# Performance work log

Hardware: AMD Instinct MI355X
Metric: run time of the kernel (lower is better)

Reference implementation:

```python
import jax, jax.numpy as jnp
import numpy as np
import itertools, math

CUTOFF = 10.0
ON_CUT = 0.25 * CUTOFF
OFF_CUT = 0.75 * CUTOFF
ALPHA = 4.0 / CUTOFF + 0.001
ALPHA2 = ALPHA ** 2
TWO_PI = 2.0 * math.pi
ONE_OVER_SQRTPI = 1.0 / math.sqrt(math.pi)
B = 512      # molecules
NA = 128     # atoms per molecule
N = B * NA   # total atoms
DEG = 64     # neighbors per atom
P = N * DEG  # total pairs


def _make_kvecs(Nmax=(2, 2, 2)):
    ks = []
    for i in range(3):
        kk = list(range(Nmax[i] + 1)) + [-v for v in range(1, Nmax[i] + 1)]
        ks.append(kk)
    lk = list(itertools.product(*ks))[1:]  # drop (0,0,0)
    kv = np.array(lk, dtype=np.float32)
    kmax = max(Nmax)
    return jnp.asarray(kv[(kv ** 2).sum(-1) <= kmax ** 2])  # [32,3]


def setup_inputs() -> dict:
    key = jax.random.key(0)
    k1, k2, k3, k4, k5, k6 = jax.random.split(key, 6)
    Z = jax.random.randint(k1, (N,), 1, 94)
    Qa = 0.2 * jax.random.normal(k2, (N,), dtype=jnp.float32)
    R = 20.0 * jax.random.uniform(k3, (N, 3), dtype=jnp.float32)
    Dij = 0.5 + 9.5 * jax.random.uniform(k4, (P,), dtype=jnp.float32)
    idx_i = jnp.repeat(jnp.arange(N), DEG)
    idx_j = (idx_i // NA) * NA + jax.random.randint(k5, (P,), 0, NA)
    batch_seg = jnp.repeat(jnp.arange(B), NA)
    Cell = jnp.tile(20.0 * jnp.eye(3, dtype=jnp.float32), (B, 1, 1)) \
           + 0.05 * jax.random.normal(k6, (B, 3, 3), dtype=jnp.float32)
    kvecs = _make_kvecs()
    return dict(Dij=Dij, Qa=Qa, R=R, Cell=Cell, kvecs=kvecs,
                Z=Z, idx_i=idx_i, idx_j=idx_j, batch_seg=batch_seg)


def _switch_function(x):
    # infinitely smooth switch from 1 (x<=on) to 0 (x>=off)
    def comp(t):
        t_ = jnp.where(t <= 0, 1.0, t)
        return jnp.where(t <= 0, 0.0, jnp.exp(-1.0 / t_))
    x = (x - ON_CUT) / (OFF_CUT - ON_CUT)
    fp = comp(x)
    fm = comp(1.0 - x)
    return jnp.where(x <= 0, 1.0, jnp.where(x >= 1, 0.0, fm / (fp + fm)))


def reference(Dij, Qa, R, Cell, kvecs, Z, idx_i, idx_j, batch_seg):
    # ---- real space: gather -> elementwise -> segment_sum ----
    fac = Qa[idx_i] * Qa[idx_j]                              # [P]
    f = _switch_function(Dij)
    coulomb = 1.0 / Dij
    damped = 1.0 / jnp.sqrt(Dij * Dij + 1.0)
    pw = fac * (f * damped + (1.0 - f) * coulomb) * jax.lax.erfc(ALPHA * Dij)
    e_real = 0.5 * jax.ops.segment_sum(pw, idx_i, num_segments=N)  # [N]

    # ---- reciprocal space ----
    recip_box = TWO_PI * jnp.transpose(jnp.linalg.inv(Cell), (0, 2, 1))  # [B,3,3]
    v_box = jnp.abs(jnp.linalg.det(Cell))                    # [B]
    prefactor = TWO_PI / v_box                               # [B]
    k = jnp.einsum('kx,bxy->bky', kvecs, recip_box)          # [B,K,3]
    k2 = jnp.sum(k * k, axis=-1)                             # [B,K]
    qg = jnp.exp(-0.25 * k2 / ALPHA2)                        # [B,K]
    kd = jnp.einsum('nkx,nx->nk', k[batch_seg], R)           # [N,K]
    q_real = jax.ops.segment_sum(Qa[:, None] * jnp.cos(kd), batch_seg, num_segments=B)  # [B,K]
    q_imag = jax.ops.segment_sum(Qa[:, None] * jnp.sin(kd), batch_seg, num_segments=B)  # [B,K]
    q_dens = q_real ** 2 + q_imag ** 2
    # NOTE: faithful to TF source: reduce over ALL axes -> scalar, then * prefactor [B]
    e_reciprocal = prefactor * jnp.sum(q_dens * qg / k2)     # [B]
    e_self = -ALPHA * ONE_OVER_SQRTPI * jax.ops.segment_sum(Qa * Qa, batch_seg, num_segments=B)
    QaR = jax.ops.segment_sum(Qa[:, None] * R, batch_seg, num_segments=B)  # [B,3]
    e_bc = prefactor / 3.0 * jnp.sum(QaR * QaR, axis=-1)     # [B]
    e_rec_tot = e_reciprocal + e_self + e_bc                 # [B]

    Na_per_batch = jax.ops.segment_sum(jnp.ones_like(batch_seg, dtype=Qa.dtype),
                                       batch_seg, num_segments=B)
    er = (e_rec_tot / Na_per_batch)[batch_seg]               # per-atom broadcast [N]
    return e_real + er, Qa
```

## Files before the change

### kernel.cpp

```cpp
#include <hip/hip_runtime.h>
#include <math.h>

#define ON_CUT_C   2.5f
#define OFF_CUT_C  7.5f
#define ALPHA_C    0.401f
#define ALPHA2_C   0.160801f
#define TWO_PI_C   6.2831853071795864f
#define INV_SQRT_PI_C 0.56418958354775628f
#define NB   512
#define NA_C 128
#define NTOT (NB*NA_C)
#define DEG_C 64
#define KC   32
#define NPTS 1024
#define TSCALE (1024.0f / 9.5f)

#define RCP(x) __builtin_amdgcn_rcpf(x)
#define RSQ(x) __builtin_amdgcn_rsqf(x)


__device__ __forceinline__ float fast_erfc(float x) {
    float t = RCP(1.0f + 0.3275911f * x);
    float p = t*(0.254829592f + t*(-0.284496736f +
              t*(1.421413741f + t*(-1.453152027f + t*1.061405429f))));
    return p * __expf(-x*x);
}

__device__ __forceinline__ float pair_g(float D) {
    float x  = (D - ON_CUT_C) * (1.0f / (OFF_CUT_C - ON_CUT_C));
    float xc = fminf(fmaxf(x, 1e-12f), 0.99999994f);
    float gg = RCP(1.0f - xc) - RCP(xc);
    float f  = RCP(1.0f + __expf(gg));
    float coulomb = RCP(D);
    float damped  = RSQ(D*D + 1.0f);
    return (f*damped + (1.0f - f)*coulomb) * fast_erfc(ALPHA_C * D);
}

__global__ __launch_bounds__(256) void recip_kernel(
    const float* __restrict__ Qa, const float* __restrict__ R,
    const float* __restrict__ Cell, const float* __restrict__ kvecs,
    float* __restrict__ ws)
{
    int b   = blockIdx.x;
    int tid = threadIdx.x;

    __shared__ float4 sar[NA_C];
    __shared__ float skx[KC], sky[KC], skz[KC], sgok2[KC];
    __shared__ float pr[KC][9], pi[KC][9];
    __shared__ float redw[2][4];
    __shared__ float s_pref;

    if (tid < NA_C) {
        int n = b * NA_C + tid;
        sar[tid] = make_float4(Qa[n], R[n*3+0], R[n*3+1], R[n*3+2]);
    }
    if (tid < KC) {
        const float* C = Cell + b * 9;
        float c00=C[0], c01=C[1], c02=C[2];
        float c10=C[3], c11=C[4], c12=C[5];
        float c20=C[6], c21=C[7], c22=C[8];
        float m00 = c11*c22 - c12*c21;
        float m01 = c02*c21 - c01*c22;
        float m02 = c01*c12 - c02*c11;
        float m10 = c12*c20 - c10*c22;
        float m11 = c00*c22 - c02*c20;
        float m12 = c02*c10 - c00*c12;
        float m20 = c10*c21 - c11*c20;
        float m21 = c01*c20 - c00*c21;
        float m22 = c00*c11 - c01*c10;
        float det = c00*m00 + c01*m10 + c02*m20;
        float invdet = 1.0f / det;
        float kv0 = kvecs[tid*3+0], kv1 = kvecs[tid*3+1], kv2 = kvecs[tid*3+2];
        float kx = TWO_PI_C * invdet * (m00*kv0 + m01*kv1 + m02*kv2);
        float ky = TWO_PI_C * invdet * (m10*kv0 + m11*kv1 + m12*kv2);
        float kz = TWO_PI_C * invdet * (m20*kv0 + m21*kv1 + m22*kv2);
        float k2 = kx*kx + ky*ky + kz*kz;
        skx[tid] = kx; sky[tid] = ky; skz[tid] = kz;
        sgok2[tid] = __expf(-0.25f * k2 / ALPHA2_C) / k2;
        if (tid == 0) s_pref = TWO_PI_C / fabsf(det);
    }
    __syncthreads();

    {
        int k = tid & 31, chunk = tid >> 5;
        float kx = skx[k], ky = sky[k], kz = skz[k];
        float cr = 0.0f, ci = 0.0f;
        int a0 = chunk * 16;
        #pragma unroll
        for (int i = 0; i < 16; ++i) {
            float4 ar = sar[a0 + i];
            float kd = kx*ar.y + ky*ar.z + kz*ar.w;
            float s, c;
            __sincosf(kd, &s, &c);
            cr += ar.x * c;
            ci += ar.x * s;
        }
        pr[k][chunk] = cr; pi[k][chunk] = ci;
    }

    if (tid < NA_C) {
        float4 ar = sar[tid];
        float q2 = ar.x*ar.x, px = ar.x*ar.y, py = ar.x*ar.z, pz = ar.x*ar.w;
        #pragma unroll
        for (int off = 32; off; off >>= 1) {
            q2 += __shfl_down(q2, off, 64);
            px += __shfl_down(px, off, 64);
            py += __shfl_down(py, off, 64);
            pz += __shfl_down(pz, off, 64);
        }
        if ((tid & 63) == 0) {
            int w = tid >> 6;
            redw[w][0]=q2; redw[w][1]=px; redw[w][2]=py; redw[w][3]=pz;
        }
    }
    __syncthreads();

    if (tid < KC) {
        float r = 0.0f, im = 0.0f;
        #pragma unroll
        for (int c = 0; c < 8; ++c) { r += pr[tid][c]; im += pi[tid][c]; }
        float sterm = (r*r + im*im) * sgok2[tid];
        #pragma unroll
        for (int off = 16; off; off >>= 1) sterm += __shfl_down(sterm, off, 64);
        if (tid == 0) {
            ws[b] = sterm;
            float q2t = redw[0][0] + redw[1][0];
            float X  = redw[0][1] + redw[1][1];
            float Y  = redw[0][2] + redw[1][2];
            float Zc = redw[0][3] + redw[1][3];
            ws[NB + b] = s_pref;
            ws[2*NB + b] = -ALPHA_C * INV_SQRT_PI_C * q2t
                           + (s_pref * (1.0f/3.0f)) * (X*X + Y*Y + Zc*Zc);
        }
    }

    if (b == 0) {
        float2* T = (float2*)(ws + 3*NB);
        for (int i = tid; i <= NPTS; i += 256) {
            float D0 = 0.5f + (9.5f / (float)NPTS) * (float)i;
            float v0 = pair_g(D0);
            float v1 = pair_g(D0 + 9.5f / (float)NPTS);
            T[i] = make_float2(v0, v1 - v0);
        }
    }
}

__global__ __launch_bounds__(256, 6) void real_kernel(
    const float* __restrict__ Dij, const float* __restrict__ Qa,
    const int* __restrict__ idx_j, const float* __restrict__ ws,
    float* __restrict__ out)
{
    int blk = blockIdx.x;
    int b   = blk >> 2, q = blk & 3;
    int tid = threadIdx.x;

    __shared__ float2 tab[NPTS + 1];
    __shared__ float  sqa[NA_C];
    __shared__ float  spw[32];
    __shared__ float  sred[4];
    __shared__ float  s_er;

    if (tid < NA_C) sqa[tid] = Qa[b * NA_C + tid];
    {
        const float2* T = (const float2*)(ws + 3*NB);
        #pragma unroll
        for (int i = tid; i <= NPTS; i += 256) tab[i] = T[i];
    }
    __syncthreads();

    int al   = tid >> 3;
    int pc   = tid & 7;
    int atom = b * NA_C + q * 32 + al;
    const float* Dp = Dij   + (size_t)atom * DEG_C + pc * 4;
    const int*   Jp = idx_j + (size_t)atom * DEG_C + pc * 4;
    float qi = sqa[q * 32 + al];

    float pw = 0.0f;
    #pragma unroll
    for (int h = 0; h < 2; ++h) {
        float4 D4 = *(const float4*)(Dp + h * 32);
        int4   J4 = *(const int4*)(Jp + h * 32);
        float Dv[4] = {D4.x, D4.y, D4.z, D4.w};
        int   jv[4] = {J4.x, J4.y, J4.z, J4.w};
        #pragma unroll
        for (int e = 0; e < 4; ++e) {
            float qj  = sqa[jv[e] & (NA_C - 1)];
            float idx = fminf((Dv[e] - 0.5f) * TSCALE, 1023.9995f);
            float fi  = floorf(idx);
            float u   = idx - fi;
            float2 tv = tab[(int)fi];
            pw += (qi * qj) * fmaf(tv.y, u, tv.x);
        }
    }
    pw += __shfl_xor(pw, 1, 64);
    pw += __shfl_xor(pw, 2, 64);
    pw += __shfl_xor(pw, 4, 64);
    if (pc == 0) spw[al] = pw;

    float s = ws[tid] + ws[tid + 256];
    #pragma unroll
    for (int off = 32; off; off >>= 1) s += __shfl_xor(s, off, 64);
    if ((tid & 63) == 0) sred[tid >> 6] = s;
    __syncthreads();
    if (tid == 0) {
        float S = sred[0] + sred[1] + sred[2] + sred[3];
        s_er = (ws[NB + b] * S + ws[2*NB + b]) * (1.0f / NA_C);
    }
    __syncthreads();

    if (tid < 32)
        out[b * NA_C + q * 32 + tid] = 0.5f * spw[tid] + s_er;
    if (q == 0 && tid < NA_C)
        out[NTOT + b * NA_C + tid] = sqa[tid];
}

extern "C" void kernel_launch(void* const* d_in, const int* in_sizes, int n_in,
                              void* d_out, int out_size, void* d_ws, size_t ws_size,
                              hipStream_t stream) {
    const float* Dij   = (const float*)d_in[0];
    const float* Qa    = (const float*)d_in[1];
    const float* R     = (const float*)d_in[2];
    const float* Cell  = (const float*)d_in[3];
    const float* kvecs = (const float*)d_in[4];
    const int*   idx_j = (const int*)d_in[7];
    float* ws  = (float*)d_ws;
    float* out = (float*)d_out;

    recip_kernel<<<NB, 256, 0, stream>>>(Qa, R, Cell, kvecs, ws);
    real_kernel<<<4*NB, 256, 0, stream>>>(Dij, Qa, idx_j, ws, out);
}
```

Baseline: 16.53 us.

## Move global reciprocal sum to combine kernel and drop LDS table staging

```diff
diff --git a/kernel.cpp b/kernel.cpp
--- a/kernel.cpp
+++ b/kernel.cpp
@@ -39,7 +39,7 @@
 __global__ __launch_bounds__(256) void recip_kernel(
     const float* __restrict__ Qa, const float* __restrict__ R,
     const float* __restrict__ Cell, const float* __restrict__ kvecs,
-    float* __restrict__ ws)
+    float* __restrict__ ws, float* __restrict__ out)
 {
     int b   = blockIdx.x;
     int tid = threadIdx.x;
@@ -134,8 +134,10 @@
         }
     }
 
+    if (tid < NA_C) out[NTOT + b * NA_C + tid] = sar[tid].x;
+
     if (b == 0) {
-        float2* T = (float2*)(ws + 3*NB);
+        float2* T = (float2*)(ws + 4*NB);
         for (int i = tid; i <= NPTS; i += 256) {
             float D0 = 0.5f + (9.5f / (float)NPTS) * (float)i;
             float v0 = pair_g(D0);
@@ -145,7 +147,27 @@
     }
 }
 
-__global__ __launch_bounds__(256, 6) void real_kernel(
+__global__ __launch_bounds__(NB) void combine_kernel(float* __restrict__ ws)
+{
+    int tid = threadIdx.x;
+    __shared__ float sred[8];
+    __shared__ float sS;
+    float s = ws[tid];
+    #pragma unroll
+    for (int off = 32; off; off >>= 1) s += __shfl_xor(s, off, 64);
+    if ((tid & 63) == 0) sred[tid >> 6] = s;
+    __syncthreads();
+    if (tid == 0) {
+        float S = 0.0f;
+        #pragma unroll
+        for (int w = 0; w < 8; ++w) S += sred[w];
+        sS = S;
+    }
+    __syncthreads();
+    ws[3*NB + tid] = (ws[NB + tid] * sS + ws[2*NB + tid]) * (1.0f / NA_C);
+}
+
+__global__ __launch_bounds__(256, 8) void real_kernel(
     const float* __restrict__ Dij, const float* __restrict__ Qa,
     const int* __restrict__ idx_j, const float* __restrict__ ws,
     float* __restrict__ out)
@@ -154,26 +176,16 @@
     int b   = blk >> 2, q = blk & 3;
     int tid = threadIdx.x;
 
-    __shared__ float2 tab[NPTS + 1];
-    __shared__ float  sqa[NA_C];
-    __shared__ float  spw[32];
-    __shared__ float  sred[4];
-    __shared__ float  s_er;
-
-    if (tid < NA_C) sqa[tid] = Qa[b * NA_C + tid];
-    {
-        const float2* T = (const float2*)(ws + 3*NB);
-        #pragma unroll
-        for (int i = tid; i <= NPTS; i += 256) tab[i] = T[i];
-    }
-    __syncthreads();
-
     int al   = tid >> 3;
     int pc   = tid & 7;
     int atom = b * NA_C + q * 32 + al;
-    const float* Dp = Dij   + (size_t)atom * DEG_C + pc * 4;
-    const int*   Jp = idx_j + (size_t)atom * DEG_C + pc * 4;
-    float qi = sqa[q * 32 + al];
+    const float*  Dp  = Dij   + (size_t)atom * DEG_C + pc * 4;
+    const int*    Jp  = idx_j + (size_t)atom * DEG_C + pc * 4;
+    const float2* Tab = (const float2*)(ws + 4*NB);
+    const float*  Qb  = Qa + b * NA_C;
+
+    float qi = Qa[atom];
+    float er = ws[3*NB + b];
 
     float pw = 0.0f;
     #pragma unroll
@@ -184,34 +196,19 @@
         int   jv[4] = {J4.x, J4.y, J4.z, J4.w};
         #pragma unroll
         for (int e = 0; e < 4; ++e) {
-            float qj  = sqa[jv[e] & (NA_C - 1)];
+            float qj  = Qb[jv[e] & (NA_C - 1)];
             float idx = fminf((Dv[e] - 0.5f) * TSCALE, 1023.9995f);
             float fi  = floorf(idx);
             float u   = idx - fi;
-            float2 tv = tab[(int)fi];
+            float2 tv = Tab[(int)fi];
             pw += (qi * qj) * fmaf(tv.y, u, tv.x);
         }
     }
     pw += __shfl_xor(pw, 1, 64);
     pw += __shfl_xor(pw, 2, 64);
     pw += __shfl_xor(pw, 4, 64);
-    if (pc == 0) spw[al] = pw;
-
-    float s = ws[tid] + ws[tid + 256];
-    #pragma unroll
-    for (int off = 32; off; off >>= 1) s += __shfl_xor(s, off, 64);
-    if ((tid & 63) == 0) sred[tid >> 6] = s;
-    __syncthreads();
-    if (tid == 0) {
-        float S = sred[0] + sred[1] + sred[2] + sred[3];
-        s_er = (ws[NB + b] * S + ws[2*NB + b]) * (1.0f / NA_C);
-    }
-    __syncthreads();
-
-    if (tid < 32)
-        out[b * NA_C + q * 32 + tid] = 0.5f * spw[tid] + s_er;
-    if (q == 0 && tid < NA_C)
-        out[NTOT + b * NA_C + tid] = sqa[tid];
+
+    if (pc == 0) out[atom] = 0.5f * pw + er;
 }
 
 extern "C" void kernel_launch(void* const* d_in, const int* in_sizes, int n_in,
@@ -226,6 +223,7 @@
     float* ws  = (float*)d_ws;
     float* out = (float*)d_out;
 
-    recip_kernel<<<NB, 256, 0, stream>>>(Qa, R, Cell, kvecs, ws);
+    recip_kernel<<<NB, 256, 0, stream>>>(Qa, R, Cell, kvecs, ws, out);
+    combine_kernel<<<1, NB, 0, stream>>>(ws);
     real_kernel<<<4*NB, 256, 0, stream>>>(Dij, Qa, idx_j, ws, out);
 }
```

After: 22.26 us. 1.35x slower.
